# Kernel optimization log

Hardware: AMD Instinct MI355X
Metric: run time of the kernel (lower is better)

Reference implementation:

```python
import jax, jax.numpy as jnp
import numpy as np

THRESHOLDS = (0.25, 0.375, 0.5, 0.625)
NUM_CLASSES = 5
SMOOTH = 1e-5  # dice smoothing constant


def setup_inputs() -> dict:
    key = jax.random.key(0)
    k1, k2 = jax.random.split(key)
    # [N, T, C, H, W]; input has 5 class channels, target 1 intensity channel
    inp = jax.random.uniform(k1, (4, 10, 5, 384, 384), dtype=jnp.float32)
    tgt = jax.random.uniform(k2, (4, 10, 1, 384, 384), dtype=jnp.float32)
    weight = jnp.array([1.0, 1.0, 2.0, 5.0, 10.0], dtype=jnp.float32)
    return {"input": inp, "target": tgt, "weight": weight}


def reference(input, target, weight):
    # permute to [N, C, T, H, W]
    x = jnp.transpose(input, (0, 2, 1, 3, 4))   # [N,5,T,H,W]
    t = jnp.transpose(target, (0, 2, 1, 3, 4))  # [N,1,T,H,W]
    # threshold binning: class index = number of thresholds <= target value
    cls = jnp.zeros(t.shape, dtype=jnp.int32)
    for thr in THRESHOLDS:
        cls = cls + (t >= thr).astype(jnp.int32)
    # one-hot scatter along class dim -> [N,5,T,H,W]
    class_ids = jnp.arange(NUM_CLASSES, dtype=jnp.int32).reshape(1, NUM_CLASSES, 1, 1, 1)
    onehot = (cls == class_ids).astype(x.dtype)
    # per-class dice over all remaining dims
    axes = (0, 2, 3, 4)
    inter = jnp.sum(x * onehot, axis=axes)                      # [5]
    denom = jnp.sum(x, axis=axes) + jnp.sum(onehot, axis=axes)  # [5]
    dice_loss = 1.0 - (2.0 * inter + SMOOTH) / (denom + SMOOTH)  # [5]
    return jnp.sum(weight * dice_loss)
```

## Files before the change

kernel.cpp:

```cpp
#include <hip/hip_runtime.h>

#define HW      147456
#define NC      5
#define NT      40
#define GX      144
#define NBLK    (GX * NT)
#define SMOOTH  1e-5f

__global__ __launch_bounds__(256) void dice_main(const float* __restrict__ inp,
                                                 const float* __restrict__ tgt,
                                                 float* __restrict__ part) {
    const int nt = blockIdx.y;
    const int hw = (blockIdx.x * 256 + threadIdx.x) << 2;

    const float4 t4 = *reinterpret_cast<const float4*>(tgt + (size_t)nt * HW + hw);

    const float* base = inp + (size_t)nt * (NC * HW) + hw;
    const float4 x0 = *reinterpret_cast<const float4*>(base);
    const float4 x1 = *reinterpret_cast<const float4*>(base + HW);
    const float4 x2 = *reinterpret_cast<const float4*>(base + 2 * HW);
    const float4 x3 = *reinterpret_cast<const float4*>(base + 3 * HW);
    const float4 x4 = *reinterpret_cast<const float4*>(base + 4 * HW);

    const int c0 = (t4.x >= 0.25f) + (t4.x >= 0.375f) + (t4.x >= 0.5f) + (t4.x >= 0.625f);
    const int c1 = (t4.y >= 0.25f) + (t4.y >= 0.375f) + (t4.y >= 0.5f) + (t4.y >= 0.625f);
    const int c2 = (t4.z >= 0.25f) + (t4.z >= 0.375f) + (t4.z >= 0.5f) + (t4.z >= 0.625f);
    const int c3 = (t4.w >= 0.25f) + (t4.w >= 0.375f) + (t4.w >= 0.5f) + (t4.w >= 0.625f);

    const float4 xs[NC] = {x0, x1, x2, x3, x4};
    float v[15];
    #pragma unroll
    for (int c = 0; c < NC; ++c) {
        const float4 x = xs[c];
        v[c] = (x.x + x.y) + (x.z + x.w);
        float iv = 0.f;
        if (c0 == c) iv += x.x;
        if (c1 == c) iv += x.y;
        if (c2 == c) iv += x.z;
        if (c3 == c) iv += x.w;
        v[5 + c]  = iv;
        v[10 + c] = (float)((c0 == c) + (c1 == c) + (c2 == c) + (c3 == c));
    }

    #pragma unroll
    for (int j = 0; j < 15; ++j) {
        #pragma unroll
        for (int off = 32; off > 0; off >>= 1)
            v[j] += __shfl_down(v[j], off, 64);
    }

    __shared__ float sm[4][15];
    const int lane = threadIdx.x & 63;
    const int wv   = threadIdx.x >> 6;
    if (lane == 0) {
        #pragma unroll
        for (int j = 0; j < 15; ++j) sm[wv][j] = v[j];
    }
    __syncthreads();
    if (threadIdx.x < 16) {
        float s = 0.f;
        if (threadIdx.x < 15)
            s = sm[0][threadIdx.x] + sm[1][threadIdx.x] +
                sm[2][threadIdx.x] + sm[3][threadIdx.x];
        part[(blockIdx.y * GX + blockIdx.x) * 16 + threadIdx.x] = s;
    }
}

__global__ __launch_bounds__(256) void dice_reduce(const float* __restrict__ part,
                                                   const float* __restrict__ w,
                                                   float* __restrict__ out) {
    const int j  = threadIdx.x & 15;
    const int rg = threadIdx.x >> 4;
    float s0 = 0.f, s1 = 0.f, s2 = 0.f, s3 = 0.f;
    for (int r = rg; r < NBLK; r += 64) {
        s0 += part[(r)      * 16 + j];
        s1 += part[(r + 16) * 16 + j];
        s2 += part[(r + 32) * 16 + j];
        s3 += part[(r + 48) * 16 + j];
    }
    const float s = (s0 + s1) + (s2 + s3);

    __shared__ float sm[16][17];
    __shared__ float tot[16];
    sm[rg][j] = s;
    __syncthreads();
    if (threadIdx.x < 16) {
        float t = 0.f;
        #pragma unroll
        for (int k = 0; k < 16; ++k) t += sm[k][threadIdx.x];
        tot[threadIdx.x] = t;
    }
    __syncthreads();
    if (threadIdx.x == 0) {
        float loss = 0.f;
        #pragma unroll
        for (int c = 0; c < NC; ++c) {
            const float inter = tot[5 + c];
            const float denom = tot[c] + tot[10 + c];
            loss += w[c] * (1.f - (2.f * inter + SMOOTH) / (denom + SMOOTH));
        }
        out[0] = loss;
    }
}

extern "C" void kernel_launch(void* const* d_in, const int* in_sizes, int n_in,
                              void* d_out, int out_size, void* d_ws, size_t ws_size,
                              hipStream_t stream) {
    const float* inp = (const float*)d_in[0];
    const float* tgt = (const float*)d_in[1];
    const float* wgt = (const float*)d_in[2];
    float* out = (float*)d_out;
    float* ws  = (float*)d_ws;

    dim3 grid(GX, NT);
    dice_main<<<grid, 256, 0, stream>>>(inp, tgt, ws);
    dice_reduce<<<1, 256, 0, stream>>>(ws, wgt, out);
}
```

Baseline: 211.4 us.

## Process four float4 groups per thread with nontemporal loads, fewer blocks

Result: faster. 199.4 us (-5.7%).

```diff
diff --git a/kernel.cpp b/kernel.cpp
--- a/kernel.cpp
+++ b/kernel.cpp
@@ -3,43 +3,56 @@
 #define HW      147456
 #define NC      5
 #define NT      40
-#define GX      144
+#define GX      36
 #define NBLK    (GX * NT)
 #define SMOOTH  1e-5f
+
+typedef float vfloat4 __attribute__((ext_vector_type(4)));
 
 __global__ __launch_bounds__(256) void dice_main(const float* __restrict__ inp,
                                                  const float* __restrict__ tgt,
                                                  float* __restrict__ part) {
-    const int nt = blockIdx.y;
-    const int hw = (blockIdx.x * 256 + threadIdx.x) << 2;
+    const int nt  = blockIdx.y;
+    const int hw0 = blockIdx.x * 4096 + (threadIdx.x << 2);
 
-    const float4 t4 = *reinterpret_cast<const float4*>(tgt + (size_t)nt * HW + hw);
+    const float* tb = tgt + (size_t)nt * HW + hw0;
+    const float* xb = inp + (size_t)nt * (NC * HW) + hw0;
 
-    const float* base = inp + (size_t)nt * (NC * HW) + hw;
-    const float4 x0 = *reinterpret_cast<const float4*>(base);
-    const float4 x1 = *reinterpret_cast<const float4*>(base + HW);
-    const float4 x2 = *reinterpret_cast<const float4*>(base + 2 * HW);
-    const float4 x3 = *reinterpret_cast<const float4*>(base + 3 * HW);
-    const float4 x4 = *reinterpret_cast<const float4*>(base + 4 * HW);
+    vfloat4 t4[4];
+    vfloat4 x4[4][NC];
+    #pragma unroll
+    for (int g = 0; g < 4; ++g)
+        t4[g] = __builtin_nontemporal_load(reinterpret_cast<const vfloat4*>(tb + g * 1024));
+    #pragma unroll
+    for (int g = 0; g < 4; ++g)
+        #pragma unroll
+        for (int c = 0; c < NC; ++c)
+            x4[g][c] = __builtin_nontemporal_load(
+                reinterpret_cast<const vfloat4*>(xb + (size_t)c * HW + g * 1024));
 
-    const int c0 = (t4.x >= 0.25f) + (t4.x >= 0.375f) + (t4.x >= 0.5f) + (t4.x >= 0.625f);
-    const int c1 = (t4.y >= 0.25f) + (t4.y >= 0.375f) + (t4.y >= 0.5f) + (t4.y >= 0.625f);
-    const int c2 = (t4.z >= 0.25f) + (t4.z >= 0.375f) + (t4.z >= 0.5f) + (t4.z >= 0.625f);
-    const int c3 = (t4.w >= 0.25f) + (t4.w >= 0.375f) + (t4.w >= 0.5f) + (t4.w >= 0.625f);
-
-    const float4 xs[NC] = {x0, x1, x2, x3, x4};
     float v[15];
     #pragma unroll
-    for (int c = 0; c < NC; ++c) {
-        const float4 x = xs[c];
-        v[c] = (x.x + x.y) + (x.z + x.w);
-        float iv = 0.f;
-        if (c0 == c) iv += x.x;
-        if (c1 == c) iv += x.y;
-        if (c2 == c) iv += x.z;
-        if (c3 == c) iv += x.w;
-        v[5 + c]  = iv;
-        v[10 + c] = (float)((c0 == c) + (c1 == c) + (c2 == c) + (c3 == c));
+    for (int j = 0; j < 15; ++j) v[j] = 0.f;
+
+    #pragma unroll
+    for (int g = 0; g < 4; ++g) {
+        const vfloat4 t = t4[g];
+        const int c0 = (t.x >= 0.25f) + (t.x >= 0.375f) + (t.x >= 0.5f) + (t.x >= 0.625f);
+        const int c1 = (t.y >= 0.25f) + (t.y >= 0.375f) + (t.y >= 0.5f) + (t.y >= 0.625f);
+        const int c2 = (t.z >= 0.25f) + (t.z >= 0.375f) + (t.z >= 0.5f) + (t.z >= 0.625f);
+        const int c3 = (t.w >= 0.25f) + (t.w >= 0.375f) + (t.w >= 0.5f) + (t.w >= 0.625f);
+        #pragma unroll
+        for (int c = 0; c < NC; ++c) {
+            const vfloat4 x = x4[g][c];
+            v[c] += (x.x + x.y) + (x.z + x.w);
+            float iv = 0.f;
+            if (c0 == c) iv += x.x;
+            if (c1 == c) iv += x.y;
+            if (c2 == c) iv += x.z;
+            if (c3 == c) iv += x.w;
+            v[5 + c]  += iv;
+            v[10 + c] += (float)((c0 == c) + (c1 == c) + (c2 == c) + (c3 == c));
+        }
     }
 
     #pragma unroll
@@ -71,14 +84,9 @@
                                                    float* __restrict__ out) {
     const int j  = threadIdx.x & 15;
     const int rg = threadIdx.x >> 4;
-    float s0 = 0.f, s1 = 0.f, s2 = 0.f, s3 = 0.f;
-    for (int r = rg; r < NBLK; r += 64) {
-        s0 += part[(r)      * 16 + j];
-        s1 += part[(r + 16) * 16 + j];
-        s2 += part[(r + 32) * 16 + j];
-        s3 += part[(r + 48) * 16 + j];
-    }
-    const float s = (s0 + s1) + (s2 + s3);
+    float s = 0.f;
+    for (int r = rg; r < NBLK; r += 16)
+        s += part[r * 16 + j];
 
     __shared__ float sm[16][17];
     __shared__ float tot[16];
```
